# Performance work log

Hardware: AMD Instinct MI355X
Metric: run time of the kernel (lower is better)

## Reference

```python
import jax, jax.numpy as jnp
import numpy as np

jax.config.update("jax_enable_x64", True)

B, S = 256, 256
TINY = float(np.finfo(np.float64).tiny)  # torch.finfo().tiny for double


def _matrix_tree_logZ(scores, mask):
    """scores: [B,S,S] float64, mask: [B,S] bool (col 0 is False).
    Returns sum over batch of log partition function (Matrix-Tree theorem)."""
    lens = mask.sum(-1)  # token counts per sentence (excludes root col)
    mask_r = mask.at[:, 0].set(True)  # index_fill(1, 0, 1)
    pair = mask_r[:, :, None] & mask_r[:, None, :]  # [B,S,S]
    s = jnp.where(pair, scores, -jnp.inf)
    m = jnp.max(s.reshape(s.shape[0], -1), axis=-1)  # [B] per-batch max for stability
    A = jnp.maximum(jnp.exp(s - m[:, None, None]), TINY)  # clamp like torch
    idx = jnp.arange(S)
    D = jnp.zeros_like(A).at[:, idx, idx].set(A.sum(-1))  # degree matrix
    eye = jnp.eye(S, dtype=A.dtype)
    # masked_scatter_: rows with mask_r True take (D - A) rows, else identity
    L = jnp.where(mask_r[:, :, None], D - A, eye)
    logZ = jnp.linalg.slogdet(L[:, 1:, 1:])[1] + m * lens
    return logZ.sum()


def setup_inputs() -> dict:
    key = jax.random.key(0)
    k1, k2 = jax.random.split(key)
    scores = jax.random.normal(k1, (B, S, S), dtype=jnp.float32)
    lens = jax.random.randint(k2, (B,), S // 2, S)  # sentence lengths
    pos = jnp.arange(S)
    # col 0 (pseudo root) False, padding beyond length False
    mask = (pos[None, :] >= 1) & (pos[None, :] < lens[:, None])
    return {"scores": scores, "mask": mask}


def reference(scores, mask):
    # mbr=True path: marginals = d logZ / d scores (computed in double like torch)
    s64 = scores.astype(jnp.float64)
    probs = jax.grad(_matrix_tree_logZ)(s64, mask)
    return probs.astype(jnp.float32)
```

## Files before the change

kernel.cpp:

```cpp
#include <hip/hip_runtime.h>
#include <math.h>


#define S 256
#define BB 256

typedef double f64x4 __attribute__((ext_vector_type(4)));

__device__ __forceinline__ int rowmap(int lr, int kb) {
    int rt = lr >> 6;
    int rb = rt + (rt >= kb ? 1 : 0);
    return rb * 64 + (lr & 63);
}

__global__ __launch_bounds__(256) void k_max(const float* __restrict__ sc,
                                             float* __restrict__ partial) {
    int b = blockIdx.y, rg = blockIdx.x;
    const float4* p4 = (const float4*)(sc + (size_t)b * S * S + rg * 8192);
    int tid = threadIdx.x;
    float4 v[8];
    #pragma unroll
    for (int it = 0; it < 8; ++it) v[it] = p4[tid + 256 * it];
    float m = -1e30f;
    #pragma unroll
    for (int it = 0; it < 8; ++it)
        m = fmaxf(m, fmaxf(fmaxf(v[it].x, v[it].y), fmaxf(v[it].z, v[it].w)));
    for (int off = 32; off > 0; off >>= 1) m = fmaxf(m, __shfl_down(m, off));
    __shared__ float sm[4];
    if ((tid & 63) == 0) sm[tid >> 6] = m;
    __syncthreads();
    if (tid == 0) partial[b * 8 + rg] = fmaxf(fmaxf(sm[0], sm[1]), fmaxf(sm[2], sm[3]));
}

__global__ void k_n(const unsigned char* __restrict__ mk, const float* __restrict__ partial,
                    double* __restrict__ mb, int* __restrict__ nb) {
    int b = blockIdx.x, j = threadIdx.x;
    __shared__ int shc[4];

    const unsigned int* mw = (const unsigned int*)mk;
    unsigned int w0 = mw[0], w1 = mw[1];
    int mode = (w0 != 0u) ? 0 : ((w1 != 0u) ? 1 : 2);

    int c;
    if (mode == 0)      c = (mk[(size_t)b * S + j] != 0);
    else if (mode == 1) c = (((const int*)mk)[(size_t)b * S + j] != 0);
    else                c = (((const long long*)mk)[(size_t)b * S + j] != 0LL);

    int lane = j & 63, wid = j >> 6;
    int cs = c;
    for (int off = 32; off > 0; off >>= 1) cs += __shfl_down(cs, off);
    if (lane == 0) shc[wid] = cs;
    __syncthreads();
    if (j == 0) {
        nb[b] = shc[0] + shc[1] + shc[2] + shc[3];
        float mm = partial[b * 8];
        #pragma unroll
        for (int q = 1; q < 8; ++q) mm = fmaxf(mm, partial[b * 8 + q]);
        mb[b] = (double)mm;
    }
}

__global__ __launch_bounds__(256) void k_build(const float* __restrict__ sc,
                                               const double* __restrict__ mb,
                                               const int* __restrict__ nb,
                                               double* __restrict__ Mg) {
    int b = blockIdx.y;
    int wid = threadIdx.x >> 6, lane = threadIdx.x & 63;
    int p = blockIdx.x * 4 + wid;
    int n = nb[b];
    double m = mb[b];
    __shared__ double se[4][260];
    double* Mrow = Mg + ((size_t)b * S + p) * S;
    bool act = (p < n);
    double ssum = 0.0;
    #pragma unroll
    for (int c4 = 0; c4 < 4; ++c4) {
        int j = lane + 64 * c4;
        double ev = 0.0;
        if (act && j <= n)
            ev = (double)expf((float)((double)sc[((size_t)b * S + (p + 1)) * S + j] - m));
        se[wid][j] = ev;
        ssum += ev;
    }
    for (int off = 32; off > 0; off >>= 1) ssum += __shfl_down(ssum, off);
    ssum = __shfl(ssum, 0);
    __syncthreads();
    #pragma unroll
    for (int c4 = 0; c4 < 4; ++c4) {
        int j = lane + 64 * c4;
        double v;
        if (act && j < n) v = ((j == p) ? ssum : 0.0) - se[wid][j + 1];
        else              v = (j == p) ? 1.0 : 0.0;
        Mrow[j] = v;
    }
}

__global__ __launch_bounds__(512) void k_step(double* __restrict__ Mg, int kb) {
    int b = blockIdx.x;
    double* M = Mg + (size_t)b * S * S;
    int tid = threadIdx.x;
    __shared__ double H[64 * 256];
    __shared__ double SCR[3104];
    __shared__ int rowtab[16];

    int pl = tid & 63;
    int pli = pl & 15, plk = pl >> 4;
    {
        f64x4 pr = {0.0, 0.0, 0.0, 0.0}, pc = {0.0, 0.0, 0.0, 0.0};
        pr = __builtin_amdgcn_mfma_f64_16x16x4f64((plk == 0) ? (double)(pli + 1) : 0.0,
                                                  (plk == 0 && pli == 0) ? 1.0 : 0.0,
                                                  pr, 0, 0, 0);
        pc = __builtin_amdgcn_mfma_f64_16x16x4f64((plk == 0) ? 1.0 : 0.0,
                                                  (plk == 0) ? (double)(pli + 1) : 0.0,
                                                  pc, 0, 0, 0);
        int cof = (int)pc[0] - 1;
        if (cof == 0) {
            #pragma unroll
            for (int v = 0; v < 4; ++v) rowtab[plk * 4 + v] = (int)pr[v] - 1;
        }
    }

    int i = tid >> 3, g = tid & 7, c0 = g << 3;
    double c[8];
    {
        const double* src = M + (size_t)(kb * 64 + i) * S + kb * 64 + c0;
        #pragma unroll
        for (int m2 = 0; m2 < 4; ++m2) {
            double2 t = *(const double2*)(src + 2 * m2);
            c[2 * m2] = t.x; c[2 * m2 + 1] = t.y;
        }
    }
    double* rbuf = SCR;
    double* cbuf = SCR + 128;
    if (i == 0) {
        #pragma unroll
        for (int u = 0; u < 8; ++u) rbuf[c0 + u] = c[u];
    }
    if (g == 0) cbuf[i] = c[0];
    for (int k = 0; k < 64; ++k) {
        int par = k & 1;
        __syncthreads();
        double pv = rbuf[par * 64 + k];
        double f  = cbuf[par * 64 + i];
        double rk[8];
        #pragma unroll
        for (int m2 = 0; m2 < 4; ++m2) {
            double2 t = *(const double2*)&rbuf[par * 64 + c0 + 2 * m2];
            rk[2 * m2] = t.x; rk[2 * m2 + 1] = t.y;
        }
        double pivinv = 1.0 / pv;
        int kg = k >> 3, ks = k & 7;
        if (i == k) {
            #pragma unroll
            for (int u = 0; u < 8; ++u)
                c[u] = ((g == kg) && (u == ks)) ? pivinv : c[u] * pivinv;
        } else {
            double gm = f * pivinv;
            #pragma unroll
            for (int u = 0; u < 8; ++u)
                c[u] = ((g == kg) && (u == ks)) ? (-gm) : fma(-gm, rk[u], c[u]);
        }
        int k1 = k + 1;
        if (k1 < 64) {
            if (i == k1) {
                #pragma unroll
                for (int u = 0; u < 8; ++u) rbuf[(par ^ 1) * 64 + c0 + u] = c[u];
            }
            if (g == (k1 >> 3)) cbuf[(par ^ 1) * 64 + i] = c[k1 & 7];
        }
    }
    __syncthreads();

    int tx = tid & 31, ty = tid >> 5;
    double* PT = SCR;
    double* Rc = SCR + 512;
    double2 ga[4][3];
    #pragma unroll
    for (int r = 0; r < 4; ++r)
        #pragma unroll
        for (int q = 0; q < 3; ++q) ga[r][q] = double2{0.0, 0.0};

    for (int cs = 0; cs < 8; ++cs) {
        if (g == cs) {
            #pragma unroll
            for (int u = 0; u < 8; ++u) PT[u * 64 + i] = c[u];
        }
        #pragma unroll
        for (int rep = 0; rep < 3; ++rep) {
            int idx = rep * 512 + tid;
            int sL = idx / 192, jj = idx - sL * 192;
            Rc[sL * 192 + jj] = M[(size_t)(kb * 64 + cs * 8 + sL) * S + rowmap(jj, kb)];
        }
        __syncthreads();
        #pragma unroll
        for (int sL = 0; sL < 8; ++sL) {
            double2 p01 = *(const double2*)&PT[sL * 64 + 4 * ty];
            double2 p23 = *(const double2*)&PT[sL * 64 + 4 * ty + 2];
            double2 r0 = *(const double2*)&Rc[sL * 192 + 2 * tx];
            double2 r1 = *(const double2*)&Rc[sL * 192 + 2 * tx + 64];
            double2 r2 = *(const double2*)&Rc[sL * 192 + 2 * tx + 128];
            ga[0][0].x = fma(p01.x, r0.x, ga[0][0].x); ga[0][0].y = fma(p01.x, r0.y, ga[0][0].y);
            ga[0][1].x = fma(p01.x, r1.x, ga[0][1].x); ga[0][1].y = fma(p01.x, r1.y, ga[0][1].y);
            ga[0][2].x = fma(p01.x, r2.x, ga[0][2].x); ga[0][2].y = fma(p01.x, r2.y, ga[0][2].y);
            ga[1][0].x = fma(p01.y, r0.x, ga[1][0].x); ga[1][0].y = fma(p01.y, r0.y, ga[1][0].y);
            ga[1][1].x = fma(p01.y, r1.x, ga[1][1].x); ga[1][1].y = fma(p01.y, r1.y, ga[1][1].y);
            ga[1][2].x = fma(p01.y, r2.x, ga[1][2].x); ga[1][2].y = fma(p01.y, r2.y, ga[1][2].y);
            ga[2][0].x = fma(p23.x, r0.x, ga[2][0].x); ga[2][0].y = fma(p23.x, r0.y, ga[2][0].y);
            ga[2][1].x = fma(p23.x, r1.x, ga[2][1].x); ga[2][1].y = fma(p23.x, r1.y, ga[2][1].y);
            ga[2][2].x = fma(p23.x, r2.x, ga[2][2].x); ga[2][2].y = fma(p23.x, r2.y, ga[2][2].y);
            ga[3][0].x = fma(p23.y, r0.x, ga[3][0].x); ga[3][0].y = fma(p23.y, r0.y, ga[3][0].y);
            ga[3][1].x = fma(p23.y, r1.x, ga[3][1].x); ga[3][1].y = fma(p23.y, r1.y, ga[3][1].y);
            ga[3][2].x = fma(p23.y, r2.x, ga[3][2].x); ga[3][2].y = fma(p23.y, r2.y, ga[3][2].y);
        }
        __syncthreads();
    }
    #pragma unroll
    for (int r = 0; r < 4; ++r)
        #pragma unroll
        for (int q = 0; q < 3; ++q) {
            int col = rowmap(2 * tx + 64 * q, kb);
            *(double2*)&H[(4 * ty + r) * 256 + col] = ga[r][q];
        }
    #pragma unroll
    for (int u = 0; u < 8; ++u) H[i * 256 + kb * 64 + c0 + u] = c[u];
    __syncthreads();

    #pragma unroll
    for (int rep = 0; rep < 16; ++rep) {
        int idx = rep * 512 + tid;
        int row = idx >> 7, col2 = idx & 127;
        *(double2*)&M[(size_t)(kb * 64 + row) * S + 2 * col2] =
            *(const double2*)&H[row * 256 + 2 * col2];
    }

    {
        int wv = tid >> 6;
        int li = pli, lk = plk;
        int ct0 = 2 * wv, ct1 = 2 * wv + 1;
        bool pivw = ((wv >> 1) == kb);
        f64x4 pc2 = {0.0, 0.0, 0.0, 0.0};
        pc2 = __builtin_amdgcn_mfma_f64_16x16x4f64((lk == 0) ? 1.0 : 0.0,
                                                   (lk == 0) ? (double)(li + 1) : 0.0,
                                                   pc2, 0, 0, 0);
        int cof = (int)pc2[0] - 1;
        int r0 = rowtab[lk * 4 + 0], r1 = rowtab[lk * 4 + 1];
        int r2 = rowtab[lk * 4 + 2], r3 = rowtab[lk * 4 + 3];
        for (int rt = 0; rt < 12; ++rt) {
            const double* Fp = M + (size_t)rowmap(rt * 16 + li, kb) * S + kb * 64 + lk;
            f64x4 acc0 = {0.0, 0.0, 0.0, 0.0};
            f64x4 acc1 = {0.0, 0.0, 0.0, 0.0};
            #pragma unroll
            for (int s = 0; s < 16; ++s) {
                double a  = -Fp[4 * s];
                double b0 = H[(4 * s + lk) * 256 + 16 * ct0 + li];
                double b1 = H[(4 * s + lk) * 256 + 16 * ct1 + li];
                acc0 = __builtin_amdgcn_mfma_f64_16x16x4f64(a, b0, acc0, 0, 0, 0);
                acc1 = __builtin_amdgcn_mfma_f64_16x16x4f64(a, b1, acc1, 0, 0, 0);
            }
            size_t g0 = (size_t)rowmap(rt * 16 + r0, kb) * S;
            size_t g1 = (size_t)rowmap(rt * 16 + r1, kb) * S;
            size_t g2 = (size_t)rowmap(rt * 16 + r2, kb) * S;
            size_t g3 = (size_t)rowmap(rt * 16 + r3, kb) * S;
            if (!pivw) {
                M[g0 + 16 * ct0 + cof] += acc0[0]; M[g0 + 16 * ct1 + cof] += acc1[0];
                M[g1 + 16 * ct0 + cof] += acc0[1]; M[g1 + 16 * ct1 + cof] += acc1[1];
                M[g2 + 16 * ct0 + cof] += acc0[2]; M[g2 + 16 * ct1 + cof] += acc1[2];
                M[g3 + 16 * ct0 + cof] += acc0[3]; M[g3 + 16 * ct1 + cof] += acc1[3];
            }
            __syncthreads();
            if (pivw) {
                M[g0 + 16 * ct0 + cof] = acc0[0]; M[g0 + 16 * ct1 + cof] = acc1[0];
                M[g1 + 16 * ct0 + cof] = acc0[1]; M[g1 + 16 * ct1 + cof] = acc1[1];
                M[g2 + 16 * ct0 + cof] = acc0[2]; M[g2 + 16 * ct1 + cof] = acc1[2];
                M[g3 + 16 * ct0 + cof] = acc0[3]; M[g3 + 16 * ct1 + cof] = acc1[3];
            }
        }
    }
}

__global__ __launch_bounds__(256) void k_diag(const double* __restrict__ Mg,
                                              const float* __restrict__ sc,
                                              const double* __restrict__ mb,
                                              const int* __restrict__ nb,
                                              double* __restrict__ Dg,
                                              float* __restrict__ out) {
    int b = blockIdx.x, t = threadIdx.x;
    const double* M = Mg + (size_t)b * S * S;
    __shared__ double sd[256];
    double d = M[(size_t)t * S + t];
    sd[t] = d;
    Dg[(size_t)b * S + t] = d;
    out[(size_t)b * S * S + t] = 0.0f;
    __syncthreads();
    int n = nb[b];
    float m = (float)mb[b];
    if (t >= 1) {
        float v = 0.0f;
        if (t <= n) {
            double A = (double)expf(sc[((size_t)b * S + t) * S + 0] - m);
            v = (float)(A * sd[t - 1]);
        }
        out[((size_t)b * S + t) * S + 0] = v;
    }
}

__global__ __launch_bounds__(256) void k_xtepi(const double* __restrict__ Mg,
                                               const float* __restrict__ sc,
                                               const double* __restrict__ mb,
                                               const int* __restrict__ nb,
                                               const double* __restrict__ Dg,
                                               float* __restrict__ out) {
    int b = blockIdx.y, t = blockIdx.x;
    int r = t & 3, c = t >> 2;
    const double* M = Mg + (size_t)b * S * S;
    __shared__ float L[64][65];
    __shared__ double sdg[64];
    int tid = threadIdx.x;
    int cc = tid & 63;
    #pragma unroll
    for (int rep = 0; rep < 16; ++rep) {
        int rr = rep * 4 + (tid >> 6);
        L[rr][cc] = (float)M[(size_t)(64 * r + rr) * S + 64 * c + cc];
    }
    if (tid < 64) sdg[tid] = Dg[(size_t)b * S + 64 * c + tid];
    __syncthreads();
    int n = nb[b];
    float m = (float)mb[b];
    int pp = tid & 63;
    #pragma unroll
    for (int rep = 0; rep < 16; ++rep) {
        int qq = rep * 4 + (tid >> 6);
        int orow = 64 * c + qq + 1, ocol = 64 * r + pp + 1;
        if (orow < 256 && ocol < 256) {
            float v = 0.0f;
            if (orow <= n && ocol <= n) {
                double A = (double)expf(sc[((size_t)b * S + orow) * S + ocol] - m);
                v = (float)(A * (sdg[qq] - (double)L[pp][qq]));
            }
            out[((size_t)b * S + orow) * S + ocol] = v;
        }
    }
}

extern "C" void kernel_launch(void* const* d_in, const int* in_sizes, int n_in,
                              void* d_out, int out_size, void* d_ws, size_t ws_size,
                              hipStream_t stream) {
    (void)in_sizes; (void)n_in; (void)out_size; (void)ws_size;
    const float* sc = (const float*)d_in[0];
    const unsigned char* mk = (const unsigned char*)d_in[1];
    double* ws = (double*)d_ws;

    double* M  = ws;
    double* mb = M + (size_t)BB * S * S;
    int*    nb = (int*)(mb + BB);
    double* Dg = mb + 2 * BB;
    float*  partial = (float*)Dg;
    float*  out = (float*)d_out;

    k_max<<<dim3(8, BB), 256, 0, stream>>>(sc, partial);
    k_n<<<BB, 256, 0, stream>>>(mk, partial, mb, nb);
    k_build<<<dim3(64, BB), 256, 0, stream>>>(sc, mb, nb, M);
    for (int kb = 0; kb < 4; ++kb)
        k_step<<<BB, 512, 0, stream>>>(M, kb);
    k_diag<<<BB, 256, 0, stream>>>(M, sc, mb, nb, Dg, out);
    k_xtepi<<<dim3(16, BB), 256, 0, stream>>>(M, sc, mb, nb, Dg, out);
}
```

Before: 579.6 us.

## Compute pivot-row panel product with FP64 MFMA and pad shared H rows

Replaces the scalar-FMA panel product (the inverted 64x64 pivot block times the pivot rows, staged through shared scratch in 8 chunks with two barriers each) with FP64 MFMA 16x16x4 tiles. These read the pivot block from shared H and the pivot rows straight from global memory, then write into H. The shared H row stride is padded from 256 to 258 doubles to reduce bank conflicts, and the scratch buffer shrinks. This removes the staging loop and its many syncthreads, at the cost of uncoalesced global reads of the pivot rows and a changed per-wave tile assignment.

```diff
diff --git a/kernel.cpp b/kernel.cpp
--- a/kernel.cpp
+++ b/kernel.cpp
@@ -4,6 +4,7 @@
 
 #define S 256
 #define BB 256
+#define HS 258
 
 typedef double f64x4 __attribute__((ext_vector_type(4)));
 
@@ -99,12 +100,13 @@
     int b = blockIdx.x;
     double* M = Mg + (size_t)b * S * S;
     int tid = threadIdx.x;
-    __shared__ double H[64 * 256];
-    __shared__ double SCR[3104];
+    __shared__ double H[64 * HS];
+    __shared__ double SCR[256];
     __shared__ int rowtab[16];
 
     int pl = tid & 63;
     int pli = pl & 15, plk = pl >> 4;
+    int cof;
     {
         f64x4 pr = {0.0, 0.0, 0.0, 0.0}, pc = {0.0, 0.0, 0.0, 0.0};
         pr = __builtin_amdgcn_mfma_f64_16x16x4f64((plk == 0) ? (double)(pli + 1) : 0.0,
@@ -113,7 +115,7 @@
         pc = __builtin_amdgcn_mfma_f64_16x16x4f64((plk == 0) ? 1.0 : 0.0,
                                                   (plk == 0) ? (double)(pli + 1) : 0.0,
                                                   pc, 0, 0, 0);
-        int cof = (int)pc[0] - 1;
+        cof = (int)pc[0] - 1;
         if (cof == 0) {
             #pragma unroll
             for (int v = 0; v < 4; ++v) rowtab[plk * 4 + v] = (int)pr[v] - 1;
@@ -169,60 +171,48 @@
             if (g == (k1 >> 3)) cbuf[(par ^ 1) * 64 + i] = c[k1 & 7];
         }
     }
-    __syncthreads();
-
-    int tx = tid & 31, ty = tid >> 5;
-    double* PT = SCR;
-    double* Rc = SCR + 512;
-    double2 ga[4][3];
-    #pragma unroll
-    for (int r = 0; r < 4; ++r)
-        #pragma unroll
-        for (int q = 0; q < 3; ++q) ga[r][q] = double2{0.0, 0.0};
-
-    for (int cs = 0; cs < 8; ++cs) {
-        if (g == cs) {
-            #pragma unroll
-            for (int u = 0; u < 8; ++u) PT[u * 64 + i] = c[u];
-        }
-        #pragma unroll
-        for (int rep = 0; rep < 3; ++rep) {
-            int idx = rep * 512 + tid;
-            int sL = idx / 192, jj = idx - sL * 192;
-            Rc[sL * 192 + jj] = M[(size_t)(kb * 64 + cs * 8 + sL) * S + rowmap(jj, kb)];
-        }
-        __syncthreads();
-        #pragma unroll
-        for (int sL = 0; sL < 8; ++sL) {
-            double2 p01 = *(const double2*)&PT[sL * 64 + 4 * ty];
-            double2 p23 = *(const double2*)&PT[sL * 64 + 4 * ty + 2];
-            double2 r0 = *(const double2*)&Rc[sL * 192 + 2 * tx];
-            double2 r1 = *(const double2*)&Rc[sL * 192 + 2 * tx + 64];
-            double2 r2 = *(const double2*)&Rc[sL * 192 + 2 * tx + 128];
-            ga[0][0].x = fma(p01.x, r0.x, ga[0][0].x); ga[0][0].y = fma(p01.x, r0.y, ga[0][0].y);
-            ga[0][1].x = fma(p01.x, r1.x, ga[0][1].x); ga[0][1].y = fma(p01.x, r1.y, ga[0][1].y);
-            ga[0][2].x = fma(p01.x, r2.x, ga[0][2].x); ga[0][2].y = fma(p01.x, r2.y, ga[0][2].y);
-            ga[1][0].x = fma(p01.y, r0.x, ga[1][0].x); ga[1][0].y = fma(p01.y, r0.y, ga[1][0].y);
-            ga[1][1].x = fma(p01.y, r1.x, ga[1][1].x); ga[1][1].y = fma(p01.y, r1.y, ga[1][1].y);
-            ga[1][2].x = fma(p01.y, r2.x, ga[1][2].x); ga[1][2].y = fma(p01.y, r2.y, ga[1][2].y);
-            ga[2][0].x = fma(p23.x, r0.x, ga[2][0].x); ga[2][0].y = fma(p23.x, r0.y, ga[2][0].y);
-            ga[2][1].x = fma(p23.x, r1.x, ga[2][1].x); ga[2][1].y = fma(p23.x, r1.y, ga[2][1].y);
-            ga[2][2].x = fma(p23.x, r2.x, ga[2][2].x); ga[2][2].y = fma(p23.x, r2.y, ga[2][2].y);
-            ga[3][0].x = fma(p23.y, r0.x, ga[3][0].x); ga[3][0].y = fma(p23.y, r0.y, ga[3][0].y);
-            ga[3][1].x = fma(p23.y, r1.x, ga[3][1].x); ga[3][1].y = fma(p23.y, r1.y, ga[3][1].y);
-            ga[3][2].x = fma(p23.y, r2.x, ga[3][2].x); ga[3][2].y = fma(p23.y, r2.y, ga[3][2].y);
-        }
-        __syncthreads();
-    }
-    #pragma unroll
-    for (int r = 0; r < 4; ++r)
-        #pragma unroll
-        for (int q = 0; q < 3; ++q) {
-            int col = rowmap(2 * tx + 64 * q, kb);
-            *(double2*)&H[(4 * ty + r) * 256 + col] = ga[r][q];
-        }
-    #pragma unroll
-    for (int u = 0; u < 8; ++u) H[i * 256 + kb * 64 + c0 + u] = c[u];
+    #pragma unroll
+    for (int u = 0; u < 8; ++u) H[i * HS + kb * 64 + c0 + u] = c[u];
+    __syncthreads();
+
+    int r0 = rowtab[plk * 4 + 0], r1 = rowtab[plk * 4 + 1];
+    int r2 = rowtab[plk * 4 + 2], r3 = rowtab[plk * 4 + 3];
+    int wv = tid >> 6;
+    int li = pli, lk = plk;
+
+    for (int grp = 0; grp < 2; ++grp) {
+        int t0 = (grp * 3 + 0) * 8 + wv, t1 = (grp * 3 + 1) * 8 + wv, t2 = (grp * 3 + 2) * 8 + wv;
+        int rtA = t0 / 12, clA = t0 % 12;
+        int rtB = t1 / 12, clB = t1 % 12;
+        int rtC = t2 / 12, clC = t2 % 12;
+        int rmA = rowmap(clA * 16, kb), rmB = rowmap(clB * 16, kb), rmC = rowmap(clC * 16, kb);
+        f64x4 aA = {0.0, 0.0, 0.0, 0.0};
+        f64x4 aB = {0.0, 0.0, 0.0, 0.0};
+        f64x4 aC = {0.0, 0.0, 0.0, 0.0};
+        #pragma unroll
+        for (int s = 0; s < 16; ++s) {
+            int kk = 4 * s + lk;
+            const double* Rrow = M + (size_t)(kb * 64 + kk) * S;
+            double pA = H[(rtA * 16 + li) * HS + kb * 64 + kk];
+            double pB = H[(rtB * 16 + li) * HS + kb * 64 + kk];
+            double pC = H[(rtC * 16 + li) * HS + kb * 64 + kk];
+            aA = __builtin_amdgcn_mfma_f64_16x16x4f64(pA, Rrow[rmA + li], aA, 0, 0, 0);
+            aB = __builtin_amdgcn_mfma_f64_16x16x4f64(pB, Rrow[rmB + li], aB, 0, 0, 0);
+            aC = __builtin_amdgcn_mfma_f64_16x16x4f64(pC, Rrow[rmC + li], aC, 0, 0, 0);
+        }
+        H[(rtA * 16 + r0) * HS + rmA + cof] = aA[0];
+        H[(rtA * 16 + r1) * HS + rmA + cof] = aA[1];
+        H[(rtA * 16 + r2) * HS + rmA + cof] = aA[2];
+        H[(rtA * 16 + r3) * HS + rmA + cof] = aA[3];
+        H[(rtB * 16 + r0) * HS + rmB + cof] = aB[0];
+        H[(rtB * 16 + r1) * HS + rmB + cof] = aB[1];
+        H[(rtB * 16 + r2) * HS + rmB + cof] = aB[2];
+        H[(rtB * 16 + r3) * HS + rmB + cof] = aB[3];
+        H[(rtC * 16 + r0) * HS + rmC + cof] = aC[0];
+        H[(rtC * 16 + r1) * HS + rmC + cof] = aC[1];
+        H[(rtC * 16 + r2) * HS + rmC + cof] = aC[2];
+        H[(rtC * 16 + r3) * HS + rmC + cof] = aC[3];
+    }
     __syncthreads();
 
     #pragma unroll
@@ -230,21 +220,12 @@
         int idx = rep * 512 + tid;
         int row = idx >> 7, col2 = idx & 127;
         *(double2*)&M[(size_t)(kb * 64 + row) * S + 2 * col2] =
-            *(const double2*)&H[row * 256 + 2 * col2];
+            *(const double2*)&H[row * HS + 2 * col2];
     }
 
     {
-        int wv = tid >> 6;
-        int li = pli, lk = plk;
         int ct0 = 2 * wv, ct1 = 2 * wv + 1;
         bool pivw = ((wv >> 1) == kb);
-        f64x4 pc2 = {0.0, 0.0, 0.0, 0.0};
-        pc2 = __builtin_amdgcn_mfma_f64_16x16x4f64((lk == 0) ? 1.0 : 0.0,
-                                                   (lk == 0) ? (double)(li + 1) : 0.0,
-                                                   pc2, 0, 0, 0);
-        int cof = (int)pc2[0] - 1;
-        int r0 = rowtab[lk * 4 + 0], r1 = rowtab[lk * 4 + 1];
-        int r2 = rowtab[lk * 4 + 2], r3 = rowtab[lk * 4 + 3];
         for (int rt = 0; rt < 12; ++rt) {
             const double* Fp = M + (size_t)rowmap(rt * 16 + li, kb) * S + kb * 64 + lk;
             f64x4 acc0 = {0.0, 0.0, 0.0, 0.0};
@@ -252,8 +233,8 @@
             #pragma unroll
             for (int s = 0; s < 16; ++s) {
                 double a  = -Fp[4 * s];
-                double b0 = H[(4 * s + lk) * 256 + 16 * ct0 + li];
-                double b1 = H[(4 * s + lk) * 256 + 16 * ct1 + li];
+                double b0 = H[(4 * s + lk) * HS + 16 * ct0 + li];
+                double b1 = H[(4 * s + lk) * HS + 16 * ct1 + li];
                 acc0 = __builtin_amdgcn_mfma_f64_16x16x4f64(a, b0, acc0, 0, 0, 0);
                 acc1 = __builtin_amdgcn_mfma_f64_16x16x4f64(a, b1, acc1, 0, 0, 0);
             }
```

Result: faster. 553.0 us (-4.6%).
